# Optimization experiments

Measured on AMD Instinct MI355X. Metric: run time of the kernel, lower is better.

The kernel has to match this reference:

```python
import jax, jax.numpy as jnp
import numpy as np

MG = (5, 5)          # mesh_grid_size
UP = (17, 17)        # upsample_size
IMG = (512.0, 512.0) # image_size
B = 8192
FC_OUT = MG[0] * MG[1] * 2  # 50
KH = (UP[0] - 1) // (MG[0] - 1) + 1  # 5
KW = (UP[1] - 1) // (MG[1] - 1) + 1  # 5
SH = (UP[0] - 1) // (MG[0] - 1)      # 4
SW = (UP[1] - 1) // (MG[1] - 1)      # 4
L0 = MG[0] - 1
L1 = MG[1] - 1


def _grid(h, w):
    # channel 0: x coords vary along rows (image_size[0]); channel 1: y along cols
    x_t = jnp.broadcast_to(jnp.linspace(0.0, IMG[0], h)[:, None], (h, w))
    y_t = jnp.broadcast_to(jnp.linspace(0.0, IMG[1], w)[None, :], (h, w))
    return jnp.stack([x_t, y_t], 0)  # [2, h, w]


def _unfold22(a):
    # a: [B, 2, H, W] -> [B, (H-1)*(W-1), 4, 2]; 4 = kernel positions row-major, 2 = channel
    p = jnp.stack([a[:, :, :-1, :-1], a[:, :, :-1, 1:],
                   a[:, :, 1:, :-1], a[:, :, 1:, 1:]], axis=2)  # [B,2,4,H-1,W-1]
    return p.reshape(a.shape[0], 2, 4, -1).transpose(0, 3, 2, 1)


def _persp(src, dst):
    # exact 4-point homography solve (torchgeometry.get_perspective_transform)
    x0, y0 = src[..., 0], src[..., 1]
    u, v = dst[..., 0], dst[..., 1]
    z = jnp.zeros_like(x0)
    o = jnp.ones_like(x0)
    ax = jnp.stack([x0, y0, o, z, z, z, -u * x0, -u * y0], -1)  # [N,4,8]
    ay = jnp.stack([z, z, z, x0, y0, o, -v * x0, -v * y0], -1)
    A = jnp.concatenate([ax, ay], 1)                 # [N,8,8]
    bb = jnp.concatenate([u, v], 1)[..., None]       # [N,8,1]
    h = jnp.linalg.solve(A, bb)[..., 0]              # [N,8]
    return jnp.concatenate([h, o[:, :1]], 1).reshape(-1, 3, 3)


def setup_inputs() -> dict:
    key = jax.random.key(0)
    ks = jax.random.split(key, 4)
    def lin(k, i, o):
        return jax.random.normal(k, (i, o), jnp.float32) / jnp.sqrt(i)
    return {
        "x": jax.random.normal(ks[0], (B, 1024), jnp.float32),
        "W1": lin(ks[1], 1024, 1024), "b1": jnp.zeros((1024,), jnp.float32),
        "W2": lin(ks[2], 1024, 2048), "b2": jnp.zeros((2048,), jnp.float32),
        "W3": lin(ks[3], 2048, FC_OUT), "b3": jnp.zeros((FC_OUT,), jnp.float32),
    }


def reference(x, W1, b1, W2, b2, W3, b3):
    Bn = x.shape[0]
    h = jax.nn.relu(x @ W1 + b1)
    h = jax.nn.relu(h @ W2 + b2)
    out = (h @ W3 + b3).reshape(Bn, 2, MG[0], MG[1])  # [B,2,5,5] mesh flow

    # sparse control grid and 2x2 patch corner points
    gs = _grid(MG[0], MG[1])
    src = _unfold22(jnp.broadcast_to(gs[None], (Bn, 2, MG[0], MG[1]))).reshape(-1, 4, 2)
    flow = _unfold22(out).reshape(-1, 4, 2)
    M = _persp(src, src + flow)  # [B*16, 3, 3]

    # dense grid and its unfold2 (kernel KHxKW, stride SHxSW) patch points
    gd = _grid(UP[0], UP[1])  # [2, 17, 17]
    gi = (np.arange(L0) * SH)[:, None, None, None] + np.arange(KH)[None, None, :, None]
    gj = (np.arange(L1) * SW)[None, :, None, None] + np.arange(KW)[None, None, None, :]
    I, J = np.broadcast_arrays(gi, gj)  # [L0,L1,KH,KW]
    pts = gd[:, I, J].transpose(1, 2, 3, 4, 0).reshape(1, L0 * L1, KH * KW, 2)
    pts = jnp.broadcast_to(pts, (Bn, L0 * L1, KH * KW, 2)).reshape(Bn * L0 * L1, KH * KW, 2)

    # transform_points: homogeneous warp + perspective divide
    ph = jnp.concatenate([pts, jnp.ones(pts.shape[:-1] + (1,), pts.dtype)], -1)
    oh = jnp.einsum('nij,npj->npi', M, ph)
    warped = oh[..., :2] / oh[..., 2:3]
    warped = warped.reshape(Bn, L0, L1, KH, KW, 2)

    # Fold: scatter-accumulate overlapping patches
    fold = jnp.zeros((Bn, 2, UP[0], UP[1]), x.dtype)
    for i in range(L0):
        for j in range(L1):
            blk = warped[:, i, j].transpose(0, 3, 1, 2)  # [B,2,KH,KW]
            fold = fold.at[:, :, i * SH:i * SH + KH, j * SW:j * SW + KW].add(blk)

    # boundary rescaling exactly as the torch code: only the 5x5 crossing points
    idx = np.arange(0, UP[0], MG[0] - 1)
    X, Y = np.meshgrid(idx, idx, indexing='xy')
    fold = fold.at[:, :, X, Y].multiply(0.5)
    for (a, b) in ((0, 0), (0, UP[1] - 1), (UP[0] - 1, UP[1] - 1), (UP[0] - 1, 0)):
        fold = fold.at[:, :, a, b].multiply(2.0)

    return fold - gd[None]  # upsampled mesh flow [B,2,17,17]
```

## Files before the change

kernel.cpp:

```cpp
#include <hip/hip_runtime.h>

typedef __bf16 bf16x8 __attribute__((ext_vector_type(8)));
typedef float f32x4 __attribute__((ext_vector_type(4)));

__device__ __forceinline__ unsigned short f2bf(float f) {
  unsigned int u = __builtin_bit_cast(unsigned int, f);
  unsigned int r = (u + 0x7fffu + ((u >> 16) & 1u)) >> 16;
  return (unsigned short)r;
}

__device__ __forceinline__ float bf2f(unsigned short u) {
  unsigned int v = ((unsigned int)u) << 16;
  return __builtin_bit_cast(float, v);
}

__device__ __forceinline__ void load16_lds(const unsigned short* g, unsigned short* l) {
  __builtin_amdgcn_global_load_lds(
      (const __attribute__((address_space(1))) void*)g,
      (__attribute__((address_space(3))) void*)l, 16, 0, 0);
}

__device__ __forceinline__ void wait_vm0() {
  asm volatile("s_waitcnt vmcnt(0)" ::: "memory");
  __builtin_amdgcn_sched_barrier(0);
}
__device__ __forceinline__ void barrier_raw() {
  __builtin_amdgcn_sched_barrier(0);
  __builtin_amdgcn_s_barrier();
  __builtin_amdgcn_sched_barrier(0);
}


__global__ __launch_bounds__(256) void prepass(
    const float* __restrict__ x, const float* __restrict__ W1,
    const float* __restrict__ W2, const float* __restrict__ W3,
    unsigned short* __restrict__ xbf, unsigned short* __restrict__ w1t,
    unsigned short* __restrict__ w2t, unsigned short* __restrict__ w3t) {
  __shared__ float tile[32][33];
  const int bid = blockIdx.x;
  const int t = threadIdx.x;
  if (bid < 2048) {
    for (int i = bid * 256 + t; i < 2097152; i += 2048 * 256) {
      float4 f = ((const float4*)x)[i];
      uint2 o;
      o.x = (unsigned)f2bf(f.x) | ((unsigned)f2bf(f.y) << 16);
      o.y = (unsigned)f2bf(f.z) | ((unsigned)f2bf(f.w) << 16);
      ((uint2*)xbf)[i] = o;
    }
  } else if (bid < 3072) {
    int ti = bid - 2048;
    int n0 = (ti & 31) * 32, k0 = (ti >> 5) * 32;
    int tx = t & 31, ty = t >> 5;
    #pragma unroll
    for (int r = 0; r < 32; r += 8)
      tile[ty + r][tx] = W1[(size_t)(k0 + ty + r) * 1024 + n0 + tx];
    __syncthreads();
    #pragma unroll
    for (int r = 0; r < 32; r += 8)
      w1t[(size_t)(n0 + ty + r) * 1024 + k0 + tx] = f2bf(tile[tx][ty + r]);
  } else if (bid < 5120) {
    int ti = bid - 3072;
    int n0 = (ti & 63) * 32, k0 = (ti >> 6) * 32;
    int tx = t & 31, ty = t >> 5;
    #pragma unroll
    for (int r = 0; r < 32; r += 8)
      tile[ty + r][tx] = W2[(size_t)(k0 + ty + r) * 2048 + n0 + tx];
    __syncthreads();
    #pragma unroll
    for (int r = 0; r < 32; r += 8)
      w2t[(size_t)(n0 + ty + r) * 1024 + k0 + tx] = f2bf(tile[tx][ty + r]);
  } else {
    int idx = (bid - 5120) * 256 + t;
    int n = idx >> 11, k = idx & 2047;
    w3t[idx] = f2bf((n < 50) ? W3[(size_t)k * 50 + n] : 0.f);
  }
}


__global__ __launch_bounds__(512, 2) void gemm1_8p(
    const unsigned short* __restrict__ A,
    const unsigned short* __restrict__ Bt,
    const float* __restrict__ bias,
    unsigned short* __restrict__ C) {
  constexpr int K = 1024, N = 1024, NT = 16;
  constexpr int AEL = 256 * 64;
  constexpr int BEL = 128 * 64;
  constexpr int BUF = AEL + BEL;
  __shared__ __align__(16) unsigned short smem[2 * BUF];
  const int t = threadIdx.x;
  const int m0 = blockIdx.x * 256;
  const int n0 = blockIdx.y * 128;
  const int lane = t & 63, wv = t >> 6;
  const int l16 = lane & 15, quad = lane >> 4;
  const int wr = wv >> 1, wc = wv & 1;
  const int rb = wr * 64, cb = wc * 64;

  const int srow = t >> 3;
  const int sg = ((t & 7) ^ (srow & 7)) * 8;
  const unsigned short* Ag0 = A + (size_t)(m0 + srow) * K + sg;
  const unsigned short* Bg0 = Bt + (size_t)(n0 + srow) * K + sg;
  const int ldsO = wv * 8 * 64;

  f32x4 acc[4][4] = {};

  #pragma unroll
  for (int r = 0; r < 4; ++r)
    load16_lds(Ag0 + (size_t)(r * 64) * K, &smem[r * 4096 + ldsO]);
  #pragma unroll
  for (int r = 0; r < 2; ++r)
    load16_lds(Bg0 + (size_t)(r * 64) * K, &smem[AEL + r * 4096 + ldsO]);

  for (int kt = 0; kt < NT; ++kt) {
    unsigned short* Ls = &smem[(kt & 1) * BUF];

    wait_vm0();
    barrier_raw();

    if (kt + 1 < NT) {
      unsigned short* Ln = &smem[((kt + 1) & 1) * BUF];
      const unsigned short* An = Ag0 + (size_t)(kt + 1) * 64;
      const unsigned short* Bn = Bg0 + (size_t)(kt + 1) * 64;
      #pragma unroll
      for (int r = 0; r < 4; ++r)
        load16_lds(An + (size_t)(r * 64) * K, &Ln[r * 4096 + ldsO]);
      #pragma unroll
      for (int r = 0; r < 2; ++r)
        load16_lds(Bn + (size_t)(r * 64) * K, &Ln[AEL + r * 4096 + ldsO]);
    }

    #pragma unroll
    for (int half = 0; half < 2; ++half) {
      bf16x8 af[4], bfr[4];
      #pragma unroll
      for (int ni = 0; ni < 4; ++ni) {
        int row = cb + ni * 16 + l16;
        bfr[ni] = *(const bf16x8*)&Ls[AEL + row * 64 + ((half * 4 + quad) ^ (row & 7)) * 8];
      }
      #pragma unroll
      for (int mi = 0; mi < 4; ++mi) {
        int row = rb + mi * 16 + l16;
        af[mi] = *(const bf16x8*)&Ls[row * 64 + ((half * 4 + quad) ^ (row & 7)) * 8];
      }
      #pragma unroll
      for (int mi = 0; mi < 4; ++mi)
        #pragma unroll
        for (int ni = 0; ni < 4; ++ni)
          acc[mi][ni] = __builtin_amdgcn_mfma_f32_16x16x32_bf16(
              af[mi], bfr[ni], acc[mi][ni], 0, 0, 0);
    }
  }
  barrier_raw();

  unsigned short* Cs = smem;
  float bv[4];
  #pragma unroll
  for (int ni = 0; ni < 4; ++ni) bv[ni] = bias[n0 + cb + ni * 16 + l16];
  #pragma unroll
  for (int mi = 0; mi < 4; ++mi)
    #pragma unroll
    for (int ni = 0; ni < 4; ++ni)
      #pragma unroll
      for (int r = 0; r < 4; ++r) {
        int row = rb + mi * 16 + quad * 4 + r;
        int col = cb + ni * 16 + l16;
        int pb = (col >> 3) ^ (row & 15);
        Cs[row * 128 + pb * 8 + (col & 7)] = f2bf(fmaxf(acc[mi][ni][r] + bv[ni], 0.f));
      }
  __syncthreads();
  #pragma unroll
  for (int j = 0; j < 8; ++j) {
    int idx = j * 512 + t;
    int row = idx >> 4, cg = idx & 15;
    int pb = cg ^ (row & 15);
    *(uint4*)&C[(size_t)(m0 + row) * N + n0 + cg * 8] =
        *(const uint4*)&Cs[row * 128 + pb * 8];
  }
}


__global__ __launch_bounds__(512, 2) void gemm2_8p(
    const unsigned short* __restrict__ A,
    const unsigned short* __restrict__ Bt,
    const float* __restrict__ bias,
    const unsigned short* __restrict__ W3t,
    unsigned short* __restrict__ part) {
  constexpr int K = 1024, NT = 16;
  constexpr int AEL = 256 * 64;
  constexpr int BUF = 2 * AEL;
  __shared__ __align__(16) unsigned short smem[2 * BUF];
  const int t = threadIdx.x;
  const int m0 = blockIdx.x * 256;
  const int n0 = blockIdx.y * 256;
  const int lane = t & 63, wv = t >> 6;
  const int l16 = lane & 15, quad = lane >> 4;
  const int wr = wv >> 2, wc = wv & 3;
  const int rb = wr * 128, cb = wc * 64;

  const int srow = t >> 3;
  const int sg = ((t & 7) ^ (srow & 7)) * 8;
  const unsigned short* Ag0 = A + (size_t)(m0 + srow) * K + sg;
  const unsigned short* Bg0 = Bt + (size_t)(n0 + srow) * K + sg;
  const int ldsO = wv * 8 * 64;

  f32x4 acc[8][4] = {};

  #pragma unroll
  for (int r = 0; r < 4; ++r) {
    load16_lds(Ag0 + (size_t)(r * 64) * K, &smem[r * 4096 + ldsO]);
    load16_lds(Bg0 + (size_t)(r * 64) * K, &smem[AEL + r * 4096 + ldsO]);
  }

  for (int kt = 0; kt < NT; ++kt) {
    unsigned short* Ls = &smem[(kt & 1) * BUF];

    wait_vm0();
    barrier_raw();

    if (kt + 1 < NT) {
      unsigned short* Ln = &smem[((kt + 1) & 1) * BUF];
      const unsigned short* An = Ag0 + (size_t)(kt + 1) * 64;
      const unsigned short* Bn = Bg0 + (size_t)(kt + 1) * 64;
      #pragma unroll
      for (int r = 0; r < 4; ++r) {
        load16_lds(An + (size_t)(r * 64) * K, &Ln[r * 4096 + ldsO]);
        load16_lds(Bn + (size_t)(r * 64) * K, &Ln[AEL + r * 4096 + ldsO]);
      }
    }

    #pragma unroll
    for (int half = 0; half < 2; ++half) {
      bf16x8 bfr[4];
      #pragma unroll
      for (int ni = 0; ni < 4; ++ni) {
        int row = cb + ni * 16 + l16;
        bfr[ni] = *(const bf16x8*)&Ls[AEL + row * 64 + ((half * 4 + quad) ^ (row & 7)) * 8];
      }
      bf16x8 af[8];
      #pragma unroll
      for (int mi = 0; mi < 8; ++mi) {
        int row = rb + mi * 16 + l16;
        af[mi] = *(const bf16x8*)&Ls[row * 64 + ((half * 4 + quad) ^ (row & 7)) * 8];
      }
      #pragma unroll
      for (int mi = 0; mi < 8; ++mi)
        #pragma unroll
        for (int ni = 0; ni < 4; ++ni)
          acc[mi][ni] = __builtin_amdgcn_mfma_f32_16x16x32_bf16(
              af[mi], bfr[ni], acc[mi][ni], 0, 0, 0);
    }
  }
  barrier_raw();

  unsigned short* Cs = smem;
  float bv[4];
  #pragma unroll
  for (int ni = 0; ni < 4; ++ni) bv[ni] = bias[n0 + cb + ni * 16 + l16];
  #pragma unroll
  for (int mi = 0; mi < 8; ++mi)
    #pragma unroll
    for (int ni = 0; ni < 4; ++ni)
      #pragma unroll
      for (int r = 0; r < 4; ++r) {
        int row = rb + mi * 16 + quad * 4 + r;
        int col = cb + ni * 16 + l16;
        int pb = (col >> 3) ^ (row & 31);
        Cs[row * 256 + pb * 8 + (col & 7)] = f2bf(fmaxf(acc[mi][ni][r] + bv[ni], 0.f));
      }
  __syncthreads();

  bf16x8 bq[8][4];
  #pragma unroll
  for (int ks = 0; ks < 8; ++ks)
    #pragma unroll
    for (int nt = 0; nt < 4; ++nt)
      bq[ks][nt] = *(const bf16x8*)&W3t[(size_t)(nt * 16 + l16) * 2048 +
                                        n0 + ks * 32 + quad * 8];
  f32x4 acc2[2][4] = {};
  #pragma unroll
  for (int ks = 0; ks < 8; ++ks) {
    bf16x8 af2[2];
    #pragma unroll
    for (int mt = 0; mt < 2; ++mt) {
      int row = wv * 32 + mt * 16 + l16;
      int pb = (ks * 4 + quad) ^ (row & 31);
      af2[mt] = *(const bf16x8*)&Cs[row * 256 + pb * 8];
    }
    #pragma unroll
    for (int mt = 0; mt < 2; ++mt)
      #pragma unroll
      for (int nt = 0; nt < 4; ++nt)
        acc2[mt][nt] = __builtin_amdgcn_mfma_f32_16x16x32_bf16(
            af2[mt], bq[ks][nt], acc2[mt][nt], 0, 0, 0);
  }

  unsigned short* pp = part + (size_t)blockIdx.y * 8192 * 64;
  #pragma unroll
  for (int mt = 0; mt < 2; ++mt)
    #pragma unroll
    for (int nt = 0; nt < 4; ++nt) {
      int col = nt * 16 + l16;
      #pragma unroll
      for (int r = 0; r < 4; ++r) {
        int row = m0 + wv * 32 + mt * 16 + quad * 4 + r;
        pp[(size_t)row * 64 + col] = f2bf(acc2[mt][nt][r]);
      }
    }
}


__global__ __launch_bounds__(256) void geom_reduce(
    const unsigned short* __restrict__ part, const float* __restrict__ b3,
    float* __restrict__ outp) {
  __shared__ float s_out3[16 * 64];
  __shared__ float fold[16 * 578];
  const int t = threadIdx.x;
  const int bbase = blockIdx.x * 16;

  for (int i = t; i < 16 * 578; i += 256) fold[i] = 0.f;
  for (int i = t; i < 1024; i += 256) {
    int m = i >> 6, n = i & 63;
    size_t idx = (size_t)(bbase + m) * 64 + n;
    float v = 0.f;
    #pragma unroll
    for (int z = 0; z < 8; ++z) v += bf2f(part[idx + (size_t)z * 8192 * 64]);
    s_out3[i] = v + ((n < 50) ? b3[n] : 0.f);
  }
  __syncthreads();

  {
    const int bl = t >> 4;
    const int p = t & 15;
    const int pi = p >> 2, pj = p & 3;
    const float* o = &s_out3[bl * 64];

    float u00 = 128.f * pi       + o[pi * 5 + pj];
    float v00 = 128.f * pj       + o[25 + pi * 5 + pj];
    float u01 = 128.f * pi       + o[pi * 5 + pj + 1];
    float v01 = 128.f * (pj + 1) + o[25 + pi * 5 + pj + 1];
    float u10 = 128.f * (pi + 1) + o[(pi + 1) * 5 + pj];
    float v10 = 128.f * pj       + o[25 + (pi + 1) * 5 + pj];
    float u11 = 128.f * (pi + 1) + o[(pi + 1) * 5 + pj + 1];
    float v11 = 128.f * (pj + 1) + o[25 + (pi + 1) * 5 + pj + 1];

    float sx = u00 - u10 + u11 - u01;
    float sy = v00 - v10 + v11 - v01;
    float dx1 = u10 - u11, dx2 = u01 - u11;
    float dy1 = v10 - v11, dy2 = v01 - v11;
    float rden = 1.f / (dx1 * dy2 - dx2 * dy1);
    float g = (sx * dy2 - dx2 * sy) * rden;
    float h = (dx1 * sy - sx * dy1) * rden;
    float a = u10 - u00 + g * u10;
    float b = u01 - u00 + h * u01;
    float c = u00;
    float d = v10 - v00 + g * v10;
    float e = v01 - v00 + h * v01;
    float f = v00;

    #pragma unroll
    for (int ai = 0; ai < 5; ++ai) {
      #pragma unroll
      for (int bi = 0; bi < 5; ++bi) {
        float s = 0.25f * ai, tt = 0.25f * bi;
        float rw = 1.f / (g * s + h * tt + 1.f);
        float xx = (a * s + b * tt + c) * rw;
        float yy = (d * s + e * tt + f) * rw;
        int gi = pi * 4 + ai, gj = pj * 4 + bi;
        atomicAdd(&fold[(bl * 2 + 0) * 289 + gi * 17 + gj], xx);
        atomicAdd(&fold[(bl * 2 + 1) * 289 + gi * 17 + gj], yy);
      }
    }
  }
  __syncthreads();

  for (int i = t; i < 16 * 578; i += 256) {
    int blb = i / 578;
    int rem = i - blb * 578;
    int ch = rem / 289;
    int ij = rem - ch * 289;
    int gi = ij / 17, gj = ij - gi * 17;
    float val = fold[i];
    if ((gi % 4 == 0) && (gj % 4 == 0)) val *= 0.5f;
    if ((gi == 0 || gi == 16) && (gj == 0 || gj == 16)) val *= 2.f;
    val -= (ch == 0) ? 32.f * gi : 32.f * gj;
    outp[(size_t)(bbase + blb) * 578 + rem] = val;
  }
}


extern "C" void kernel_launch(void* const* d_in, const int* in_sizes, int n_in,
                              void* d_out, int out_size, void* d_ws, size_t ws_size,
                              hipStream_t stream) {
  const float* x  = (const float*)d_in[0];
  const float* W1 = (const float*)d_in[1];
  const float* b1 = (const float*)d_in[2];
  const float* W2 = (const float*)d_in[3];
  const float* b2 = (const float*)d_in[4];
  const float* W3 = (const float*)d_in[5];
  const float* b3 = (const float*)d_in[6];
  float* outp = (float*)d_out;

  char* ws = (char*)d_ws;
  unsigned short* xbf = (unsigned short*)ws;
  unsigned short* w1t = (unsigned short*)(ws + (size_t)16 * 1024 * 1024);
  unsigned short* part = (unsigned short*)ws;
  unsigned short* w2t = (unsigned short*)(ws + (size_t)34 * 1024 * 1024);
  unsigned short* w3t = (unsigned short*)(ws + (size_t)38 * 1024 * 1024);
  unsigned short* h1  = (unsigned short*)(ws + (size_t)38 * 1024 * 1024 + 512 * 1024);

  prepass<<<5632, 256, 0, stream>>>(x, W1, W2, W3, xbf, w1t, w2t, w3t);

  gemm1_8p<<<dim3(32, 8), 512, 0, stream>>>(xbf, w1t, b1, h1);
  gemm2_8p<<<dim3(32, 8), 512, 0, stream>>>(h1, w2t, b2, w3t, part);
  geom_reduce<<<512, 256, 0, stream>>>(part, b3, outp);
}
```

Before: 200.3 us.

## Halve GEMM workgroup size to four waves with larger per-wave tiles

Both GEMM kernels now run with 256 threads (4 waves) instead of 512 (8 waves). The block tile stays the same, so each wave computes twice as many output tiles (8x4 or 8x8 MFMA accumulators), and the global-to-LDS staging loops issue twice as many loads per thread. The aim is more register-level reuse of A/B fragments per LDS read and less barrier overhead. The cost is higher register pressure, especially the 8x8 accumulators in gemm2, and fewer waves available to hide latency.

```diff
diff --git a/kernel.cpp b/kernel.cpp
--- a/kernel.cpp
+++ b/kernel.cpp
@@ -77,7 +77,7 @@
 }
 
 
-__global__ __launch_bounds__(512, 2) void gemm1_8p(
+__global__ __launch_bounds__(256, 1) void gemm1_bw(
     const unsigned short* __restrict__ A,
     const unsigned short* __restrict__ Bt,
     const float* __restrict__ bias,
@@ -92,23 +92,22 @@
   const int n0 = blockIdx.y * 128;
   const int lane = t & 63, wv = t >> 6;
   const int l16 = lane & 15, quad = lane >> 4;
-  const int wr = wv >> 1, wc = wv & 1;
-  const int rb = wr * 64, cb = wc * 64;
+  const int rb = (wv >> 1) * 128, cb = (wv & 1) * 64;
 
   const int srow = t >> 3;
   const int sg = ((t & 7) ^ (srow & 7)) * 8;
   const unsigned short* Ag0 = A + (size_t)(m0 + srow) * K + sg;
   const unsigned short* Bg0 = Bt + (size_t)(n0 + srow) * K + sg;
-  const int ldsO = wv * 8 * 64;
-
-  f32x4 acc[4][4] = {};
-
+  const int ldsO = wv * 512;
+
+  f32x4 acc[8][4] = {};
+
+  #pragma unroll
+  for (int r = 0; r < 8; ++r)
+    load16_lds(Ag0 + (size_t)(r * 32) * K, &smem[r * 2048 + ldsO]);
   #pragma unroll
   for (int r = 0; r < 4; ++r)
-    load16_lds(Ag0 + (size_t)(r * 64) * K, &smem[r * 4096 + ldsO]);
-  #pragma unroll
-  for (int r = 0; r < 2; ++r)
-    load16_lds(Bg0 + (size_t)(r * 64) * K, &smem[AEL + r * 4096 + ldsO]);
+    load16_lds(Bg0 + (size_t)(r * 32) * K, &smem[AEL + r * 2048 + ldsO]);
 
   for (int kt = 0; kt < NT; ++kt) {
     unsigned short* Ls = &smem[(kt & 1) * BUF];
@@ -121,28 +120,28 @@
       const unsigned short* An = Ag0 + (size_t)(kt + 1) * 64;
       const unsigned short* Bn = Bg0 + (size_t)(kt + 1) * 64;
       #pragma unroll
+      for (int r = 0; r < 8; ++r)
+        load16_lds(An + (size_t)(r * 32) * K, &Ln[r * 2048 + ldsO]);
+      #pragma unroll
       for (int r = 0; r < 4; ++r)
-        load16_lds(An + (size_t)(r * 64) * K, &Ln[r * 4096 + ldsO]);
-      #pragma unroll
-      for (int r = 0; r < 2; ++r)
-        load16_lds(Bn + (size_t)(r * 64) * K, &Ln[AEL + r * 4096 + ldsO]);
+        load16_lds(Bn + (size_t)(r * 32) * K, &Ln[AEL + r * 2048 + ldsO]);
     }
 
     #pragma unroll
     for (int half = 0; half < 2; ++half) {
-      bf16x8 af[4], bfr[4];
+      bf16x8 af[8], bfr[4];
       #pragma unroll
       for (int ni = 0; ni < 4; ++ni) {
         int row = cb + ni * 16 + l16;
         bfr[ni] = *(const bf16x8*)&Ls[AEL + row * 64 + ((half * 4 + quad) ^ (row & 7)) * 8];
       }
       #pragma unroll
-      for (int mi = 0; mi < 4; ++mi) {
+      for (int mi = 0; mi < 8; ++mi) {
         int row = rb + mi * 16 + l16;
         af[mi] = *(const bf16x8*)&Ls[row * 64 + ((half * 4 + quad) ^ (row & 7)) * 8];
       }
       #pragma unroll
-      for (int mi = 0; mi < 4; ++mi)
+      for (int mi = 0; mi < 8; ++mi)
         #pragma unroll
         for (int ni = 0; ni < 4; ++ni)
           acc[mi][ni] = __builtin_amdgcn_mfma_f32_16x16x32_bf16(
@@ -156,7 +155,7 @@
   #pragma unroll
   for (int ni = 0; ni < 4; ++ni) bv[ni] = bias[n0 + cb + ni * 16 + l16];
   #pragma unroll
-  for (int mi = 0; mi < 4; ++mi)
+  for (int mi = 0; mi < 8; ++mi)
     #pragma unroll
     for (int ni = 0; ni < 4; ++ni)
       #pragma unroll
@@ -168,17 +167,17 @@
       }
   __syncthreads();
   #pragma unroll
-  for (int j = 0; j < 8; ++j) {
-    int idx = j * 512 + t;
-    int row = idx >> 4, cg = idx & 15;
-    int pb = cg ^ (row & 15);
-    *(uint4*)&C[(size_t)(m0 + row) * N + n0 + cg * 8] =
+  for (int j = 0; j < 16; ++j) {
+    int idx = j * 256 + t;
+    int row = idx >> 4, cgc = idx & 15;
+    int pb = cgc ^ (row & 15);
+    *(uint4*)&C[(size_t)(m0 + row) * N + n0 + cgc * 8] =
         *(const uint4*)&Cs[row * 128 + pb * 8];
   }
 }
 
 
-__global__ __launch_bounds__(512, 2) void gemm2_8p(
+__global__ __launch_bounds__(256, 1) void gemm2_bw(
     const unsigned short* __restrict__ A,
     const unsigned short* __restrict__ Bt,
     const float* __restrict__ bias,
@@ -193,21 +192,20 @@
   const int n0 = blockIdx.y * 256;
   const int lane = t & 63, wv = t >> 6;
   const int l16 = lane & 15, quad = lane >> 4;
-  const int wr = wv >> 2, wc = wv & 3;
-  const int rb = wr * 128, cb = wc * 64;
+  const int rb = (wv >> 1) * 128, cb = (wv & 1) * 128;
 
   const int srow = t >> 3;
   const int sg = ((t & 7) ^ (srow & 7)) * 8;
   const unsigned short* Ag0 = A + (size_t)(m0 + srow) * K + sg;
   const unsigned short* Bg0 = Bt + (size_t)(n0 + srow) * K + sg;
-  const int ldsO = wv * 8 * 64;
-
-  f32x4 acc[8][4] = {};
-
-  #pragma unroll
-  for (int r = 0; r < 4; ++r) {
-    load16_lds(Ag0 + (size_t)(r * 64) * K, &smem[r * 4096 + ldsO]);
-    load16_lds(Bg0 + (size_t)(r * 64) * K, &smem[AEL + r * 4096 + ldsO]);
+  const int ldsO = wv * 512;
+
+  f32x4 acc[8][8] = {};
+
+  #pragma unroll
+  for (int r = 0; r < 8; ++r) {
+    load16_lds(Ag0 + (size_t)(r * 32) * K, &smem[r * 2048 + ldsO]);
+    load16_lds(Bg0 + (size_t)(r * 32) * K, &smem[AEL + r * 2048 + ldsO]);
   }
 
   for (int kt = 0; kt < NT; ++kt) {
@@ -221,20 +219,14 @@
       const unsigned short* An = Ag0 + (size_t)(kt + 1) * 64;
       const unsigned short* Bn = Bg0 + (size_t)(kt + 1) * 64;
       #pragma unroll
-      for (int r = 0; r < 4; ++r) {
-        load16_lds(An + (size_t)(r * 64) * K, &Ln[r * 4096 + ldsO]);
-        load16_lds(Bn + (size_t)(r * 64) * K, &Ln[AEL + r * 4096 + ldsO]);
+      for (int r = 0; r < 8; ++r) {
+        load16_lds(An + (size_t)(r * 32) * K, &Ln[r * 2048 + ldsO]);
+        load16_lds(Bn + (size_t)(r * 32) * K, &Ln[AEL + r * 2048 + ldsO]);
       }
     }
 
     #pragma unroll
     for (int half = 0; half < 2; ++half) {
-      bf16x8 bfr[4];
-      #pragma unroll
-      for (int ni = 0; ni < 4; ++ni) {
-        int row = cb + ni * 16 + l16;
-        bfr[ni] = *(const bf16x8*)&Ls[AEL + row * 64 + ((half * 4 + quad) ^ (row & 7)) * 8];
-      }
       bf16x8 af[8];
       #pragma unroll
       for (int mi = 0; mi < 8; ++mi) {
@@ -242,23 +234,32 @@
         af[mi] = *(const bf16x8*)&Ls[row * 64 + ((half * 4 + quad) ^ (row & 7)) * 8];
       }
       #pragma unroll
-      for (int mi = 0; mi < 8; ++mi)
+      for (int nh = 0; nh < 2; ++nh) {
+        bf16x8 bfr[4];
         #pragma unroll
-        for (int ni = 0; ni < 4; ++ni)
-          acc[mi][ni] = __builtin_amdgcn_mfma_f32_16x16x32_bf16(
-              af[mi], bfr[ni], acc[mi][ni], 0, 0, 0);
+        for (int ni = 0; ni < 4; ++ni) {
+          int row = cb + nh * 64 + ni * 16 + l16;
+          bfr[ni] = *(const bf16x8*)&Ls[AEL + row * 64 + ((half * 4 + quad) ^ (row & 7)) * 8];
+        }
+        #pragma unroll
+        for (int mi = 0; mi < 8; ++mi)
+          #pragma unroll
+          for (int ni = 0; ni < 4; ++ni)
+            acc[mi][nh * 4 + ni] = __builtin_amdgcn_mfma_f32_16x16x32_bf16(
+                af[mi], bfr[ni], acc[mi][nh * 4 + ni], 0, 0, 0);
+      }
     }
   }
   barrier_raw();
 
   unsigned short* Cs = smem;
-  float bv[4];
-  #pragma unroll
-  for (int ni = 0; ni < 4; ++ni) bv[ni] = bias[n0 + cb + ni * 16 + l16];
+  float bv[8];
+  #pragma unroll
+  for (int ni = 0; ni < 8; ++ni) bv[ni] = bias[n0 + cb + ni * 16 + l16];
   #pragma unroll
   for (int mi = 0; mi < 8; ++mi)
     #pragma unroll
-    for (int ni = 0; ni < 4; ++ni)
+    for (int ni = 0; ni < 8; ++ni)
       #pragma unroll
       for (int r = 0; r < 4; ++r) {
         int row = rb + mi * 16 + quad * 4 + r;
@@ -275,18 +276,18 @@
     for (int nt = 0; nt < 4; ++nt)
       bq[ks][nt] = *(const bf16x8*)&W3t[(size_t)(nt * 16 + l16) * 2048 +
                                         n0 + ks * 32 + quad * 8];
-  f32x4 acc2[2][4] = {};
+  f32x4 acc2[4][4] = {};
   #pragma unroll
   for (int ks = 0; ks < 8; ++ks) {
-    bf16x8 af2[2];
-    #pragma unroll
-    for (int mt = 0; mt < 2; ++mt) {
-      int row = wv * 32 + mt * 16 + l16;
+    bf16x8 af2[4];
+    #pragma unroll
+    for (int mt = 0; mt < 4; ++mt) {
+      int row = wv * 64 + mt * 16 + l16;
       int pb = (ks * 4 + quad) ^ (row & 31);
       af2[mt] = *(const bf16x8*)&Cs[row * 256 + pb * 8];
     }
     #pragma unroll
-    for (int mt = 0; mt < 2; ++mt)
+    for (int mt = 0; mt < 4; ++mt)
       #pragma unroll
       for (int nt = 0; nt < 4; ++nt)
         acc2[mt][nt] = __builtin_amdgcn_mfma_f32_16x16x32_bf16(
@@ -295,13 +296,13 @@
 
   unsigned short* pp = part + (size_t)blockIdx.y * 8192 * 64;
   #pragma unroll
-  for (int mt = 0; mt < 2; ++mt)
+  for (int mt = 0; mt < 4; ++mt)
     #pragma unroll
     for (int nt = 0; nt < 4; ++nt) {
       int col = nt * 16 + l16;
       #pragma unroll
       for (int r = 0; r < 4; ++r) {
-        int row = m0 + wv * 32 + mt * 16 + quad * 4 + r;
+        int row = m0 + wv * 64 + mt * 16 + quad * 4 + r;
         pp[(size_t)row * 64 + col] = f2bf(acc2[mt][nt][r]);
       }
     }
@@ -409,7 +410,7 @@
 
   prepass<<<5632, 256, 0, stream>>>(x, W1, W2, W3, xbf, w1t, w2t, w3t);
 
-  gemm1_8p<<<dim3(32, 8), 512, 0, stream>>>(xbf, w1t, b1, h1);
-  gemm2_8p<<<dim3(32, 8), 512, 0, stream>>>(h1, w2t, b2, w3t, part);
+  gemm1_bw<<<dim3(32, 8), 256, 0, stream>>>(xbf, w1t, b1, h1);
+  gemm2_bw<<<dim3(32, 8), 256, 0, stream>>>(h1, w2t, b2, w3t, part);
   geom_reduce<<<512, 256, 0, stream>>>(part, b3, outp);
 }
```

Result: slower. 209.0 us (+4.4%).

## Replace LDS atomic fold with gather from unfolded patches; interleave split-K partials

Applied to the files above, without the earlier changes.

The geometry kernel no longer accumulates warped points into a shared fold buffer with LDS atomics. It stores each patch's 25 warped points in an unfolded shared array, and the output pass gathers the 1, 2 or 4 overlapping contributions for each grid point. Separately, the GEMM2 split-K partials are laid out row-major with the 8 z-slices adjacent, so the reduce reads them contiguously instead of strided by 8192*64. This trades atomic contention and zero-init for extra index arithmetic and branching in the final pass.

```diff
diff --git a/kernel.cpp b/kernel.cpp
--- a/kernel.cpp
+++ b/kernel.cpp
@@ -92,8 +92,7 @@
   const int n0 = blockIdx.y * 128;
   const int lane = t & 63, wv = t >> 6;
   const int l16 = lane & 15, quad = lane >> 4;
-  const int wr = wv >> 1, wc = wv & 1;
-  const int rb = wr * 64, cb = wc * 64;
+  const int rb = (wv >> 1) * 64, cb = (wv & 1) * 64;
 
   const int srow = t >> 3;
   const int sg = ((t & 7) ^ (srow & 7)) * 8;
@@ -193,8 +192,7 @@
   const int n0 = blockIdx.y * 256;
   const int lane = t & 63, wv = t >> 6;
   const int l16 = lane & 15, quad = lane >> 4;
-  const int wr = wv >> 2, wc = wv & 3;
-  const int rb = wr * 128, cb = wc * 64;
+  const int rb = (wv >> 2) * 128, cb = (wv & 3) * 64;
 
   const int srow = t >> 3;
   const int sg = ((t & 7) ^ (srow & 7)) * 8;
@@ -293,7 +291,7 @@
             af2[mt], bq[ks][nt], acc2[mt][nt], 0, 0, 0);
   }
 
-  unsigned short* pp = part + (size_t)blockIdx.y * 8192 * 64;
+  const int zi = blockIdx.y;
   #pragma unroll
   for (int mt = 0; mt < 2; ++mt)
     #pragma unroll
@@ -302,27 +300,27 @@
       #pragma unroll
       for (int r = 0; r < 4; ++r) {
         int row = m0 + wv * 32 + mt * 16 + quad * 4 + r;
-        pp[(size_t)row * 64 + col] = f2bf(acc2[mt][nt][r]);
+        part[((size_t)row * 8 + zi) * 64 + col] = f2bf(acc2[mt][nt][r]);
       }
     }
 }
 
 
 __global__ __launch_bounds__(256) void geom_reduce(
-    const unsigned short* __restrict__ part, const float* __restrict__ b3,
+    const unsigned short* __restrict__ part,
+    const float* __restrict__ b3,
     float* __restrict__ outp) {
   __shared__ float s_out3[16 * 64];
-  __shared__ float fold[16 * 578];
+  __shared__ float unfold[16][16][50];
   const int t = threadIdx.x;
   const int bbase = blockIdx.x * 16;
 
-  for (int i = t; i < 16 * 578; i += 256) fold[i] = 0.f;
   for (int i = t; i < 1024; i += 256) {
     int m = i >> 6, n = i & 63;
-    size_t idx = (size_t)(bbase + m) * 64 + n;
+    const unsigned short* p = part + ((size_t)(bbase + m) * 8) * 64 + n;
     float v = 0.f;
     #pragma unroll
-    for (int z = 0; z < 8; ++z) v += bf2f(part[idx + (size_t)z * 8192 * 64]);
+    for (int z = 0; z < 8; ++z) v += bf2f(p[z * 64]);
     s_out3[i] = v + ((n < 50) ? b3[n] : 0.f);
   }
   __syncthreads();
@@ -362,11 +360,8 @@
       for (int bi = 0; bi < 5; ++bi) {
         float s = 0.25f * ai, tt = 0.25f * bi;
         float rw = 1.f / (g * s + h * tt + 1.f);
-        float xx = (a * s + b * tt + c) * rw;
-        float yy = (d * s + e * tt + f) * rw;
-        int gi = pi * 4 + ai, gj = pj * 4 + bi;
-        atomicAdd(&fold[(bl * 2 + 0) * 289 + gi * 17 + gj], xx);
-        atomicAdd(&fold[(bl * 2 + 1) * 289 + gi * 17 + gj], yy);
+        unfold[bl][p][ai * 5 + bi]      = (a * s + b * tt + c) * rw;
+        unfold[bl][p][25 + ai * 5 + bi] = (d * s + e * tt + f) * rw;
       }
     }
   }
@@ -378,8 +373,30 @@
     int ch = rem / 289;
     int ij = rem - ch * 289;
     int gi = ij / 17, gj = ij - gi * 17;
-    float val = fold[i];
-    if ((gi % 4 == 0) && (gj % 4 == 0)) val *= 0.5f;
+
+    int pi0 = (gi == 16) ? 3 : (gi >> 2);
+    int ai0 = gi - 4 * pi0;
+    int ci = (((gi & 3) == 0) && gi != 0 && gi != 16) ? 2 : 1;
+    int pj0 = (gj == 16) ? 3 : (gj >> 2);
+    int bj0 = gj - 4 * pj0;
+    int cj = (((gj & 3) == 0) && gj != 0 && gj != 16) ? 2 : 1;
+
+    float val = 0.f;
+    #pragma unroll
+    for (int ii = 0; ii < 2; ++ii) {
+      if (ii < ci) {
+        int pi = pi0 - ii, ai = ii ? 4 : ai0;
+        #pragma unroll
+        for (int jj = 0; jj < 2; ++jj) {
+          if (jj < cj) {
+            int pj = pj0 - jj, bi = jj ? 4 : bj0;
+            val += unfold[blb][pi * 4 + pj][ch * 25 + ai * 5 + bi];
+          }
+        }
+      }
+    }
+
+    if (((gi & 3) == 0) && ((gj & 3) == 0)) val *= 0.5f;
     if ((gi == 0 || gi == 16) && (gj == 0 || gj == 16)) val *= 2.f;
     val -= (ch == 0) ? 32.f * gi : 32.f * gj;
     outp[(size_t)(bbase + blb) * 578 + rem] = val;
```

Measured after the change: 177.0 us (median of 2 runs). -11.6%, faster.
